# Optimization experiments

Hardware: AMD Instinct MI355X
Metric: run time of the kernel (lower is better)

## Reference

```python
import jax, jax.numpy as jnp
import numpy as np

B, L, D = 2, 2048, 2048
H, KV, HD = 16, 4, 64  # query heads, kv heads, head_dim
EPS = 1e-6
ROPE_BASE = 10000.0


def setup_inputs() -> dict:
    key = jax.random.key(0)
    k0, k1, k2 = jax.random.split(key, 3)
    x = jax.random.normal(k0, (B, L, D), dtype=jnp.float32)
    W_qkv = jax.random.normal(k1, ((H + 2 * KV) * HD, D), dtype=jnp.float32) * 0.02
    W_out = jax.random.normal(k2, (D, H * HD), dtype=jnp.float32) * 0.02
    q_norm_w = jnp.ones((HD,), dtype=jnp.float32)
    k_norm_w = jnp.ones((HD,), dtype=jnp.float32)
    # causal additive mask (forward's optional `mask` arg)
    mask = jnp.triu(jnp.full((L, L), -1e9, dtype=jnp.float32), k=1)
    return {"x": x, "W_qkv": W_qkv, "W_out": W_out,
            "q_norm_w": q_norm_w, "k_norm_w": k_norm_w, "mask": mask}


def _rms_norm(x, w):
    # normalize over last (head) dim
    var = jnp.mean(x * x, axis=-1, keepdims=True)
    return x * jax.lax.rsqrt(var + EPS) * w


def _rope(x):
    # x: [B, nH, L, HD]; non-traditional (rotate-half) RoPE, offset=0
    half = HD // 2
    freqs = ROPE_BASE ** (-jnp.arange(0, HD, 2, dtype=jnp.float32) / HD)  # [half]
    theta = jnp.arange(L, dtype=jnp.float32)[:, None] * freqs[None, :]    # [L, half]
    cos, sin = jnp.cos(theta), jnp.sin(theta)
    x1, x2 = x[..., :half], x[..., half:]
    return jnp.concatenate([x1 * cos - x2 * sin, x1 * sin + x2 * cos], axis=-1)


def reference(x, W_qkv, W_out, q_norm_w, k_norm_w, mask):
    # fused QKV projection
    qkv = jnp.einsum("bld,ed->ble", x, W_qkv)                       # [B,L,(H+2KV)*HD]
    qkv = qkv.reshape(B, L, H + 2 * KV, HD).transpose(0, 2, 1, 3)   # [B,nH,L,HD]
    q, k, v = jnp.split(qkv, [H, H + KV], axis=1)
    # per-head QK RMSNorm + RoPE
    q = _rope(_rms_norm(q, q_norm_w))
    k = _rope(_rms_norm(k, k_norm_w))
    # GQA: repeat kv heads to match query heads
    rep = H // KV
    k = jnp.repeat(k, rep, axis=1)
    v = jnp.repeat(v, rep, axis=1)
    scale = HD ** -0.5
    scores = jnp.einsum("bhqd,bhkd->bhqk", q, k) * scale + mask      # [B,H,L,L]
    attn = jax.nn.softmax(scores, axis=-1)
    out = jnp.einsum("bhqk,bhkd->bhqd", attn, v)                     # [B,H,L,HD]
    out = out.transpose(0, 2, 1, 3).reshape(B, L, H * HD)
    return jnp.einsum("ble,de->bld", out, W_out)                     # [B,L,D]
```

## Files before the change

### kernel.cpp

```cpp
#include <hip/hip_runtime.h>
#include <hip/hip_bf16.h>


typedef __bf16 bf16;
typedef bf16 bf16x8 __attribute__((ext_vector_type(8)));
typedef bf16 bf16x4 __attribute__((ext_vector_type(4)));
typedef float f32x4 __attribute__((ext_vector_type(4)));

#define L_SEQ 2048
#define NQH 16
#define NKVH 4

typedef __attribute__((address_space(3))) void lds_void;
typedef const __attribute__((address_space(1))) void glb_void;
__device__ __forceinline__ void async_ld16(const void* g, void* l) {
  __builtin_amdgcn_global_load_lds((glb_void*)g, (lds_void*)l, 16, 0, 0);
}

__global__ __launch_bounds__(256) void cast_bf16(const float* __restrict__ in,
                                                 bf16* __restrict__ out, int n) {
  int i = (blockIdx.x * 256 + threadIdx.x) * 4;
  if (i < n) {
    float4 v = *(const float4*)&in[i];
    bf16x4 o;
    o[0] = (bf16)v.x; o[1] = (bf16)v.y; o[2] = (bf16)v.z; o[3] = (bf16)v.w;
    *(bf16x4*)&out[i] = o;
  }
}


__global__ __launch_bounds__(256)
void gemm_bt64(const bf16* __restrict__ A, const bf16* __restrict__ B,
               float* __restrict__ C, int M, int N, int K) {
  constexpr int ASZ = 128 * 32, BSZ = 64 * 32;
  __shared__ bf16 As[2 * ASZ];
  __shared__ bf16 Bs[2 * BSZ];
  const int tid = threadIdx.x;
  const int lane = tid & 63, w = tid >> 6;
  const int lq = lane & 15, g = lane >> 4;
  const int wr = w >> 1, wc = w & 1;
  const int bx = blockIdx.x, by = blockIdx.y;

  const bf16* gA[2];
  bf16* ldsA[2];
  const bf16* gB0;
  bf16* ldsB0;
#pragma unroll
  for (int c = 0; c < 2; ++c) {
    int slot = c * 256 + tid;
    int row = slot >> 2, ch = slot & 3;
    int sch = ch ^ ((row >> 1) & 3);
    gA[c] = &A[(size_t)(by * 128 + row) * K + sch * 8];
    ldsA[c] = &As[(c * 256 + w * 64) * 8];
  }
  {
    int row = tid >> 2, ch = tid & 3;
    int sch = ch ^ ((row >> 1) & 3);
    gB0 = &B[(size_t)(bx * 64 + row) * K + sch * 8];
    ldsB0 = &Bs[(w * 64) * 8];
  }

  f32x4 acc[4][2] = {};
  const int nk = K >> 5;
  int cur = 0;

#pragma unroll
  for (int c = 0; c < 2; ++c) async_ld16(gA[c], ldsA[c]);
  async_ld16(gB0, ldsB0);
  __syncthreads();
  for (int kt = 0; kt < nk; ++kt) {
    bf16x8 af[4], bfr[2];
#pragma unroll
    for (int i = 0; i < 4; ++i) {
      int ra = wr * 64 + i * 16 + lq;
      af[i] = *(const bf16x8*)&As[cur * ASZ + ra * 32 + (g ^ ((ra >> 1) & 3)) * 8];
    }
#pragma unroll
    for (int j = 0; j < 2; ++j) {
      int rb = wc * 32 + j * 16 + lq;
      bfr[j] = *(const bf16x8*)&Bs[cur * BSZ + rb * 32 + (g ^ ((rb >> 1) & 3)) * 8];
    }
    if (kt + 1 < nk) {
#pragma unroll
      for (int c = 0; c < 2; ++c) async_ld16(gA[c] + (kt + 1) * 32, ldsA[c] + (cur ^ 1) * ASZ);
      async_ld16(gB0 + (kt + 1) * 32, ldsB0 + (cur ^ 1) * BSZ);
    }
#pragma unroll
    for (int i = 0; i < 4; ++i)
#pragma unroll
      for (int j = 0; j < 2; ++j)
        acc[i][j] = __builtin_amdgcn_mfma_f32_16x16x32_bf16(af[i], bfr[j], acc[i][j], 0, 0, 0);
    __syncthreads();
    cur ^= 1;
  }
#pragma unroll
  for (int i = 0; i < 4; ++i)
#pragma unroll
    for (int j = 0; j < 2; ++j) {
      int row = by * 128 + wr * 64 + i * 16 + g * 4;
      int col = bx * 64 + wc * 32 + j * 16 + lq;
#pragma unroll
      for (int r = 0; r < 4; ++r) C[(size_t)(row + r) * N + col] = acc[i][j][r];
    }
}

__global__ __launch_bounds__(256)
void gemm_qkv_fused(const bf16* __restrict__ A, const bf16* __restrict__ B,
                    const float* __restrict__ qw, const float* __restrict__ kw,
                    bf16* __restrict__ Qb, bf16* __restrict__ Kb,
                    bf16* __restrict__ Vt) {
  constexpr int K = 2048;
  constexpr int ASZ = 128 * 32, BSZ = 64 * 32;
  extern __shared__ char smem[];
  bf16* As = (bf16*)smem;
  bf16* Bs = (bf16*)(smem + 2 * ASZ * 2);
  float* F = (float*)smem;
  const int tid = threadIdx.x;
  const int lane = tid & 63, w = tid >> 6;
  const int lq = lane & 15, g = lane >> 4;
  const int wr = w >> 1, wc = w & 1;
  const int bx = blockIdx.x, by = blockIdx.y;

  const bf16* gA[2];
  bf16* ldsA[2];
  const bf16* gB0;
  bf16* ldsB0;
#pragma unroll
  for (int c = 0; c < 2; ++c) {
    int slot = c * 256 + tid;
    int row = slot >> 2, ch = slot & 3;
    int sch = ch ^ ((row >> 1) & 3);
    gA[c] = &A[(size_t)(by * 128 + row) * K + sch * 8];
    ldsA[c] = &As[(c * 256 + w * 64) * 8];
  }
  {
    int row = tid >> 2, ch = tid & 3;
    int sch = ch ^ ((row >> 1) & 3);
    gB0 = &B[(size_t)(bx * 64 + row) * K + sch * 8];
    ldsB0 = &Bs[(w * 64) * 8];
  }

  f32x4 acc[4][2] = {};
  constexpr int nk = K >> 5;
  int cur = 0;

#pragma unroll
  for (int c = 0; c < 2; ++c) async_ld16(gA[c], ldsA[c]);
  async_ld16(gB0, ldsB0);
  __syncthreads();
  for (int kt = 0; kt < nk; ++kt) {
    bf16x8 af[4], bfr[2];
#pragma unroll
    for (int i = 0; i < 4; ++i) {
      int ra = wr * 64 + i * 16 + lq;
      af[i] = *(const bf16x8*)&As[cur * ASZ + ra * 32 + (g ^ ((ra >> 1) & 3)) * 8];
    }
#pragma unroll
    for (int j = 0; j < 2; ++j) {
      int rb = wc * 32 + j * 16 + lq;
      bfr[j] = *(const bf16x8*)&Bs[cur * BSZ + rb * 32 + (g ^ ((rb >> 1) & 3)) * 8];
    }
    if (kt + 1 < nk) {
#pragma unroll
      for (int c = 0; c < 2; ++c) async_ld16(gA[c] + (kt + 1) * 32, ldsA[c] + (cur ^ 1) * ASZ);
      async_ld16(gB0 + (kt + 1) * 32, ldsB0 + (cur ^ 1) * BSZ);
    }
#pragma unroll
    for (int i = 0; i < 4; ++i)
#pragma unroll
      for (int j = 0; j < 2; ++j)
        acc[i][j] = __builtin_amdgcn_mfma_f32_16x16x32_bf16(af[i], bfr[j], acc[i][j], 0, 0, 0);
    __syncthreads();
    cur ^= 1;
  }

#pragma unroll
  for (int i = 0; i < 4; ++i)
#pragma unroll
    for (int j = 0; j < 2; ++j) {
      int row = wr * 64 + i * 16 + g * 4;
      int col = wc * 32 + j * 16 + lq;
#pragma unroll
      for (int r = 0; r < 4; ++r) F[(row + r) * 66 + col] = acc[i][j][r];
    }
  __syncthreads();

  const int h = bx;
  const int b = by >> 4;
  const int l0 = (by & 15) * 128;

  if (h < 20) {
    const int row = tid >> 1;
    const int half = tid & 1;
    const float* Fr = &F[row * 66];
    float ss = 0.f;
#pragma unroll
    for (int c = 0; c < 32; ++c) {
      float v = Fr[half * 32 + c];
      ss += v * v;
    }
    ss += __shfl_xor(ss, 1);
    const float rs = rsqrtf(ss * (1.f / 64.f) + 1e-6f);
    const int l = l0 + row;
    const float* wn = (h < 16) ? qw : kw;
    const float scale = (h < 16) ? 0.125f : 1.f;
    bf16 lo[16], hi[16];
#pragma unroll
    for (int k = 0; k < 16; ++k) {
      int c = half * 16 + k;
      float x1 = Fr[c] * rs * wn[c];
      float x2 = Fr[c + 32] * rs * wn[c + 32];
      float theta = (float)l * exp2f(-(float)c * 0.41524101186280154f);
      float sn, cs;
      sincosf(theta, &sn, &cs);
      lo[k] = (bf16)((x1 * cs - x2 * sn) * scale);
      hi[k] = (bf16)((x1 * sn + x2 * cs) * scale);
    }
    bf16* dst = (h < 16) ? &Qb[((size_t)(b * NQH + h) * L_SEQ + l) * 64]
                         : &Kb[((size_t)(b * NKVH + (h - 16)) * L_SEQ + l) * 64];
    *(bf16x8*)&dst[half * 16] = *(bf16x8*)&lo[0];
    *(bf16x8*)&dst[half * 16 + 8] = *(bf16x8*)&lo[8];
    *(bf16x8*)&dst[half * 16 + 32] = *(bf16x8*)&hi[0];
    *(bf16x8*)&dst[half * 16 + 40] = *(bf16x8*)&hi[8];
  } else {
    const int d = tid >> 2;
    const int lg = (tid & 3) * 32;
    bf16 tv[32];
#pragma unroll
    for (int jj = 0; jj < 32; ++jj) tv[jj] = (bf16)F[(lg + jj) * 66 + d];
    bf16* dst = &Vt[(size_t)(b * NKVH + (h - 20)) * 64 * L_SEQ + (size_t)d * L_SEQ + l0 + lg];
#pragma unroll
    for (int c = 0; c < 4; ++c) *(bf16x8*)&dst[c * 8] = *(bf16x8*)&tv[c * 8];
  }
}

__global__ __launch_bounds__(256)
void attn(const bf16* __restrict__ Qb, const bf16* __restrict__ Kb,
          const bf16* __restrict__ Vt, bf16* __restrict__ Ao) {
  const int pair = blockIdx.x;
  const int bh = blockIdx.y;
  const int b = bh >> 4, h = bh & 15, kv = h >> 2;
  const int tid = threadIdx.x;
  const int w = tid >> 6, lane = tid & 63;
  const int lq = lane & 15, g = lane >> 4;

  __shared__ bf16 Ks[64][64];
  __shared__ bf16 Vs[64][64];
  __shared__ bf16 Plds[4][16][72];

  const bf16* Qp = Qb + (size_t)(b * NQH + h) * L_SEQ * 64;
  const bf16* Kp = Kb + (size_t)(b * NKVH + kv) * L_SEQ * 64;
  const bf16* Vp = Vt + (size_t)(b * NKVH + kv) * 64 * L_SEQ;

  const int sr0 = tid >> 3, sc = tid & 7;
  const int sr1 = sr0 + 32;
  const int swc0 = (sc ^ (sr0 & 7)) * 8;
  bf16x8 rk0, rk1, rv0, rv1;

  auto load_tile = [&](int k0) {
    rk0 = *(const bf16x8*)&Kp[(size_t)(k0 + sr0) * 64 + sc * 8];
    rk1 = *(const bf16x8*)&Kp[(size_t)(k0 + sr1) * 64 + sc * 8];
    rv0 = *(const bf16x8*)&Vp[(size_t)sr0 * L_SEQ + k0 + sc * 8];
    rv1 = *(const bf16x8*)&Vp[(size_t)sr1 * L_SEQ + k0 + sc * 8];
  };
  auto write_tile = [&]() {
    *(bf16x8*)&Ks[sr0][swc0] = rk0;
    *(bf16x8*)&Ks[sr1][swc0] = rk1;
    *(bf16x8*)&Vs[sr0][swc0] = rv0;
    *(bf16x8*)&Vs[sr1][swc0] = rv1;
  };

  const float L2E = 1.4426950408889634f;

  for (int half = 0; half < 2; ++half) {
    const int qblk = half ? (31 - pair) : pair;
    const int qr0 = qblk * 64 + w * 16;
    const int qg = qr0 + lq;

    bf16x8 qf[2];
    qf[0] = *(const bf16x8*)&Qp[(qr0 + lq) * 64 + g * 8];
    qf[1] = *(const bf16x8*)&Qp[(qr0 + lq) * 64 + 32 + g * 8];

    f32x4 o[4] = {};
    float m = -1e30f, lsum = 0.f;

    const int nkt = qblk + 1;
    load_tile(0);
    __syncthreads();
    write_tile();
    __syncthreads();

    for (int kt = 0; kt < nkt; ++kt) {
      const int k0 = kt * 64;
      const bool diag = (kt == nkt - 1);
      if (kt + 1 < nkt) load_tile(k0 + 64);

      f32x4 s[4] = {};
#pragma unroll
      for (int ks = 0; ks < 4; ++ks) {
        if (!diag || ks <= w) {
          const int row = ks * 16 + lq, sw = lq & 7;
          bf16x8 kf0 = *(const bf16x8*)&Ks[row][(g ^ sw) * 8];
          bf16x8 kf1 = *(const bf16x8*)&Ks[row][((g + 4) ^ sw) * 8];
          s[ks] = __builtin_amdgcn_mfma_f32_16x16x32_bf16(kf0, qf[0], s[ks], 0, 0, 0);
          s[ks] = __builtin_amdgcn_mfma_f32_16x16x32_bf16(kf1, qf[1], s[ks], 0, 0, 0);
        }
      }
      if (diag) {
#pragma unroll
        for (int ks = 0; ks < 4; ++ks)
#pragma unroll
          for (int r = 0; r < 4; ++r)
            if (k0 + ks * 16 + g * 4 + r > qg) s[ks][r] = -1e30f;
      }
      float tmax = -1e30f;
#pragma unroll
      for (int ks = 0; ks < 4; ++ks)
#pragma unroll
        for (int r = 0; r < 4; ++r) tmax = fmaxf(tmax, s[ks][r]);
      tmax = fmaxf(tmax, __shfl_xor(tmax, 16));
      tmax = fmaxf(tmax, __shfl_xor(tmax, 32));
      float mnew = fmaxf(m, tmax);
      float alpha = exp2f((m - mnew) * L2E);
      m = mnew;
      float rsum = 0.f;
#pragma unroll
      for (int ks = 0; ks < 4; ++ks) {
        bf16x4 p;
#pragma unroll
        for (int r = 0; r < 4; ++r) {
          float pv = exp2f((s[ks][r] - mnew) * L2E);
          rsum += pv;
          p[r] = (bf16)pv;
        }
        *(bf16x4*)&Plds[w][lq][ks * 16 + g * 4] = p;
      }
      rsum += __shfl_xor(rsum, 16);
      rsum += __shfl_xor(rsum, 32);
      lsum = lsum * alpha + rsum;

      float ar[4];
#pragma unroll
      for (int r = 0; r < 4; ++r) ar[r] = __shfl(alpha, (lane & 48) | (g * 4 + r));
#pragma unroll
      for (int dt = 0; dt < 4; ++dt)
#pragma unroll
        for (int r = 0; r < 4; ++r) o[dt][r] *= ar[r];

      bf16x8 pf0 = *(const bf16x8*)&Plds[w][lq][g * 8];
      bf16x8 pf1 = *(const bf16x8*)&Plds[w][lq][32 + g * 8];
#pragma unroll
      for (int dt = 0; dt < 4; ++dt) {
        const int row = dt * 16 + lq, sw = lq & 7;
        bf16x8 vf0 = *(const bf16x8*)&Vs[row][(g ^ sw) * 8];
        o[dt] = __builtin_amdgcn_mfma_f32_16x16x32_bf16(pf0, vf0, o[dt], 0, 0, 0);
        if (!diag || w >= 2) {
          bf16x8 vf1 = *(const bf16x8*)&Vs[row][((g + 4) ^ sw) * 8];
          o[dt] = __builtin_amdgcn_mfma_f32_16x16x32_bf16(pf1, vf1, o[dt], 0, 0, 0);
        }
      }

      if (kt + 1 < nkt) {
        __syncthreads();
        write_tile();
        __syncthreads();
      }
    }

    float linv = 1.f / lsum;
#pragma unroll
    for (int r = 0; r < 4; ++r) {
      float li = __shfl(linv, (lane & 48) | (g * 4 + r));
      int row = b * L_SEQ + qr0 + g * 4 + r;
#pragma unroll
      for (int dt = 0; dt < 4; ++dt)
        Ao[(size_t)row * 1024 + h * 64 + dt * 16 + lq] = (bf16)(o[dt][r] * li);
    }
  }
}

extern "C" void kernel_launch(void* const* d_in, const int* in_sizes, int n_in,
                              void* d_out, int out_size, void* d_ws, size_t ws_size,
                              hipStream_t stream) {
  const float* x = (const float*)d_in[0];
  const float* Wqkv = (const float*)d_in[1];
  const float* Wout = (const float*)d_in[2];
  const float* qw = (const float*)d_in[3];
  const float* kw = (const float*)d_in[4];
  float* out = (float*)d_out;

  char* ws = (char*)d_ws;
  size_t off = 0;
  auto alloc = [&](size_t bytes) {
    void* p = ws + off;
    off = (off + bytes + 255) & ~(size_t)255;
    return p;
  };
  bf16* xb = (bf16*)alloc(8388608ull * 2);
  bf16* wqb = (bf16*)alloc(3145728ull * 2);
  bf16* wob = (bf16*)alloc(2097152ull * 2);
  bf16* Qb = (bf16*)alloc(4194304ull * 2);
  bf16* Kb = (bf16*)alloc(1048576ull * 2);
  bf16* Vt = (bf16*)alloc(1048576ull * 2);
  bf16* Ao = (bf16*)alloc(4194304ull * 2);

  cast_bf16<<<8192, 256, 0, stream>>>(x, xb, 8388608);
  cast_bf16<<<3072, 256, 0, stream>>>(Wqkv, wqb, 3145728);
  cast_bf16<<<2048, 256, 0, stream>>>(Wout, wob, 2097152);
  gemm_qkv_fused<<<dim3(24, 32), 256, 33792, stream>>>(xb, wqb, qw, kw, Qb, Kb, Vt);
  attn<<<dim3(16, 32), 256, 0, stream>>>(Qb, Kb, Vt, Ao);
  gemm_bt64<<<dim3(32, 32), 256, 0, stream>>>(Ao, wob, out, 4096, 2048, 1024);
}
```

Measured before the change: 271.9 us.

## Fuse fp32-to-bf16 casts into GEMM loaders and double-buffer attention K/V tiles

Removes the three standalone cast kernels: the QKV and output GEMMs now load fp32 operands into registers, convert to bf16 and store into swizzled LDS, double-buffered around the MFMA loop. The attention kernel gets double-buffered K/V LDS tiles, so each iteration needs one barrier instead of two. This drops the cast launches and the bf16 intermediate round trip. In exchange the GEMMs re-read fp32 data, twice the bytes per tile, and lose the async global-to-LDS path.

```diff
diff --git a/kernel.cpp b/kernel.cpp
--- a/kernel.cpp
+++ b/kernel.cpp
@@ -17,95 +17,15 @@
   __builtin_amdgcn_global_load_lds((glb_void*)g, (lds_void*)l, 16, 0, 0);
 }
 
-__global__ __launch_bounds__(256) void cast_bf16(const float* __restrict__ in,
-                                                 bf16* __restrict__ out, int n) {
-  int i = (blockIdx.x * 256 + threadIdx.x) * 4;
-  if (i < n) {
-    float4 v = *(const float4*)&in[i];
-    bf16x4 o;
-    o[0] = (bf16)v.x; o[1] = (bf16)v.y; o[2] = (bf16)v.z; o[3] = (bf16)v.w;
-    *(bf16x4*)&out[i] = o;
-  }
-}
-
+__device__ __forceinline__ bf16x8 cvt8(const float4& a, const float4& b) {
+  bf16x8 v;
+  v[0] = (bf16)a.x; v[1] = (bf16)a.y; v[2] = (bf16)a.z; v[3] = (bf16)a.w;
+  v[4] = (bf16)b.x; v[5] = (bf16)b.y; v[6] = (bf16)b.z; v[7] = (bf16)b.w;
+  return v;
+}
 
 __global__ __launch_bounds__(256)
-void gemm_bt64(const bf16* __restrict__ A, const bf16* __restrict__ B,
-               float* __restrict__ C, int M, int N, int K) {
-  constexpr int ASZ = 128 * 32, BSZ = 64 * 32;
-  __shared__ bf16 As[2 * ASZ];
-  __shared__ bf16 Bs[2 * BSZ];
-  const int tid = threadIdx.x;
-  const int lane = tid & 63, w = tid >> 6;
-  const int lq = lane & 15, g = lane >> 4;
-  const int wr = w >> 1, wc = w & 1;
-  const int bx = blockIdx.x, by = blockIdx.y;
-
-  const bf16* gA[2];
-  bf16* ldsA[2];
-  const bf16* gB0;
-  bf16* ldsB0;
-#pragma unroll
-  for (int c = 0; c < 2; ++c) {
-    int slot = c * 256 + tid;
-    int row = slot >> 2, ch = slot & 3;
-    int sch = ch ^ ((row >> 1) & 3);
-    gA[c] = &A[(size_t)(by * 128 + row) * K + sch * 8];
-    ldsA[c] = &As[(c * 256 + w * 64) * 8];
-  }
-  {
-    int row = tid >> 2, ch = tid & 3;
-    int sch = ch ^ ((row >> 1) & 3);
-    gB0 = &B[(size_t)(bx * 64 + row) * K + sch * 8];
-    ldsB0 = &Bs[(w * 64) * 8];
-  }
-
-  f32x4 acc[4][2] = {};
-  const int nk = K >> 5;
-  int cur = 0;
-
-#pragma unroll
-  for (int c = 0; c < 2; ++c) async_ld16(gA[c], ldsA[c]);
-  async_ld16(gB0, ldsB0);
-  __syncthreads();
-  for (int kt = 0; kt < nk; ++kt) {
-    bf16x8 af[4], bfr[2];
-#pragma unroll
-    for (int i = 0; i < 4; ++i) {
-      int ra = wr * 64 + i * 16 + lq;
-      af[i] = *(const bf16x8*)&As[cur * ASZ + ra * 32 + (g ^ ((ra >> 1) & 3)) * 8];
-    }
-#pragma unroll
-    for (int j = 0; j < 2; ++j) {
-      int rb = wc * 32 + j * 16 + lq;
-      bfr[j] = *(const bf16x8*)&Bs[cur * BSZ + rb * 32 + (g ^ ((rb >> 1) & 3)) * 8];
-    }
-    if (kt + 1 < nk) {
-#pragma unroll
-      for (int c = 0; c < 2; ++c) async_ld16(gA[c] + (kt + 1) * 32, ldsA[c] + (cur ^ 1) * ASZ);
-      async_ld16(gB0 + (kt + 1) * 32, ldsB0 + (cur ^ 1) * BSZ);
-    }
-#pragma unroll
-    for (int i = 0; i < 4; ++i)
-#pragma unroll
-      for (int j = 0; j < 2; ++j)
-        acc[i][j] = __builtin_amdgcn_mfma_f32_16x16x32_bf16(af[i], bfr[j], acc[i][j], 0, 0, 0);
-    __syncthreads();
-    cur ^= 1;
-  }
-#pragma unroll
-  for (int i = 0; i < 4; ++i)
-#pragma unroll
-    for (int j = 0; j < 2; ++j) {
-      int row = by * 128 + wr * 64 + i * 16 + g * 4;
-      int col = bx * 64 + wc * 32 + j * 16 + lq;
-#pragma unroll
-      for (int r = 0; r < 4; ++r) C[(size_t)(row + r) * N + col] = acc[i][j][r];
-    }
-}
-
-__global__ __launch_bounds__(256)
-void gemm_qkv_fused(const bf16* __restrict__ A, const bf16* __restrict__ B,
+void gemm_qkv_fused(const float* __restrict__ A32, const float* __restrict__ B32,
                     const float* __restrict__ qw, const float* __restrict__ kw,
                     bf16* __restrict__ Qb, bf16* __restrict__ Kb,
                     bf16* __restrict__ Vt) {
@@ -121,32 +41,36 @@
   const int wr = w >> 1, wc = w & 1;
   const int bx = blockIdx.x, by = blockIdx.y;
 
-  const bf16* gA[2];
-  bf16* ldsA[2];
-  const bf16* gB0;
-  bf16* ldsB0;
-#pragma unroll
-  for (int c = 0; c < 2; ++c) {
-    int slot = c * 256 + tid;
-    int row = slot >> 2, ch = slot & 3;
-    int sch = ch ^ ((row >> 1) & 3);
-    gA[c] = &A[(size_t)(by * 128 + row) * K + sch * 8];
-    ldsA[c] = &As[(c * 256 + w * 64) * 8];
-  }
-  {
-    int row = tid >> 2, ch = tid & 3;
-    int sch = ch ^ ((row >> 1) & 3);
-    gB0 = &B[(size_t)(bx * 64 + row) * K + sch * 8];
-    ldsB0 = &Bs[(w * 64) * 8];
-  }
+  const int sch = tid & 3;
+  const int srowA = tid >> 2;
+  const int srowB = tid >> 2;
+  const float* gA0 = &A32[(size_t)(by * 128 + srowA) * K + sch * 8];
+  const float* gA1 = &A32[(size_t)(by * 128 + 64 + srowA) * K + sch * 8];
+  const float* gB0 = &B32[(size_t)(bx * 64 + srowB) * K + sch * 8];
+  const int pchA = (sch ^ ((srowA >> 1) & 3)) * 8;
+  const int pchB = (sch ^ ((srowB >> 1) & 3)) * 8;
+
+  float4 ra0[2], ra1[2], rb[2];
+  auto load_regs = [&](int kt) {
+    const float* p0 = gA0 + kt * 32;
+    ra0[0] = *(const float4*)p0; ra0[1] = *(const float4*)(p0 + 4);
+    const float* p1 = gA1 + kt * 32;
+    ra1[0] = *(const float4*)p1; ra1[1] = *(const float4*)(p1 + 4);
+    const float* pb = gB0 + kt * 32;
+    rb[0] = *(const float4*)pb; rb[1] = *(const float4*)(pb + 4);
+  };
+  auto cvt_write = [&](int buf) {
+    *(bf16x8*)&As[buf * ASZ + srowA * 32 + pchA] = cvt8(ra0[0], ra0[1]);
+    *(bf16x8*)&As[buf * ASZ + (64 + srowA) * 32 + pchA] = cvt8(ra1[0], ra1[1]);
+    *(bf16x8*)&Bs[buf * BSZ + srowB * 32 + pchB] = cvt8(rb[0], rb[1]);
+  };
 
   f32x4 acc[4][2] = {};
   constexpr int nk = K >> 5;
   int cur = 0;
 
-#pragma unroll
-  for (int c = 0; c < 2; ++c) async_ld16(gA[c], ldsA[c]);
-  async_ld16(gB0, ldsB0);
+  load_regs(0);
+  cvt_write(0);
   __syncthreads();
   for (int kt = 0; kt < nk; ++kt) {
     bf16x8 af[4], bfr[2];
@@ -157,19 +81,16 @@
     }
 #pragma unroll
     for (int j = 0; j < 2; ++j) {
-      int rb = wc * 32 + j * 16 + lq;
-      bfr[j] = *(const bf16x8*)&Bs[cur * BSZ + rb * 32 + (g ^ ((rb >> 1) & 3)) * 8];
-    }
-    if (kt + 1 < nk) {
-#pragma unroll
-      for (int c = 0; c < 2; ++c) async_ld16(gA[c] + (kt + 1) * 32, ldsA[c] + (cur ^ 1) * ASZ);
-      async_ld16(gB0 + (kt + 1) * 32, ldsB0 + (cur ^ 1) * BSZ);
-    }
+      int rbr = wc * 32 + j * 16 + lq;
+      bfr[j] = *(const bf16x8*)&Bs[cur * BSZ + rbr * 32 + (g ^ ((rbr >> 1) & 3)) * 8];
+    }
+    if (kt + 1 < nk) load_regs(kt + 1);
 #pragma unroll
     for (int i = 0; i < 4; ++i)
 #pragma unroll
       for (int j = 0; j < 2; ++j)
         acc[i][j] = __builtin_amdgcn_mfma_f32_16x16x32_bf16(af[i], bfr[j], acc[i][j], 0, 0, 0);
+    if (kt + 1 < nk) cvt_write(cur ^ 1);
     __syncthreads();
     cur ^= 1;
   }
@@ -235,6 +156,82 @@
 }
 
 __global__ __launch_bounds__(256)
+void gemm_out(const bf16* __restrict__ A, const float* __restrict__ B32,
+              float* __restrict__ C, int M, int N, int K) {
+  constexpr int ASZ = 128 * 32, BSZ = 64 * 32;
+  __shared__ bf16 As[2 * ASZ];
+  __shared__ bf16 Bs[2 * BSZ];
+  const int tid = threadIdx.x;
+  const int lane = tid & 63, w = tid >> 6;
+  const int lq = lane & 15, g = lane >> 4;
+  const int wr = w >> 1, wc = w & 1;
+  const int bx = blockIdx.x, by = blockIdx.y;
+
+  const bf16* gA[2];
+  bf16* ldsA[2];
+#pragma unroll
+  for (int c = 0; c < 2; ++c) {
+    int slot = c * 256 + tid;
+    int row = slot >> 2, ch = slot & 3;
+    int sch = ch ^ ((row >> 1) & 3);
+    gA[c] = &A[(size_t)(by * 128 + row) * K + sch * 8];
+    ldsA[c] = &As[(c * 256 + w * 64) * 8];
+  }
+  const int sch = tid & 3;
+  const int srowB = tid >> 2;
+  const float* gB0 = &B32[(size_t)(bx * 64 + srowB) * K + sch * 8];
+  const int pchB = (sch ^ ((srowB >> 1) & 3)) * 8;
+  float4 rb[2];
+
+  f32x4 acc[4][2] = {};
+  const int nk = K >> 5;
+  int cur = 0;
+
+#pragma unroll
+  for (int c = 0; c < 2; ++c) async_ld16(gA[c], ldsA[c]);
+  rb[0] = *(const float4*)gB0; rb[1] = *(const float4*)(gB0 + 4);
+  *(bf16x8*)&Bs[srowB * 32 + pchB] = cvt8(rb[0], rb[1]);
+  __syncthreads();
+  for (int kt = 0; kt < nk; ++kt) {
+    bf16x8 af[4], bfr[2];
+#pragma unroll
+    for (int i = 0; i < 4; ++i) {
+      int ra = wr * 64 + i * 16 + lq;
+      af[i] = *(const bf16x8*)&As[cur * ASZ + ra * 32 + (g ^ ((ra >> 1) & 3)) * 8];
+    }
+#pragma unroll
+    for (int j = 0; j < 2; ++j) {
+      int rbr = wc * 32 + j * 16 + lq;
+      bfr[j] = *(const bf16x8*)&Bs[cur * BSZ + rbr * 32 + (g ^ ((rbr >> 1) & 3)) * 8];
+    }
+    if (kt + 1 < nk) {
+#pragma unroll
+      for (int c = 0; c < 2; ++c) async_ld16(gA[c] + (kt + 1) * 32, ldsA[c] + (cur ^ 1) * ASZ);
+      const float* pb = gB0 + (kt + 1) * 32;
+      rb[0] = *(const float4*)pb; rb[1] = *(const float4*)(pb + 4);
+    }
+#pragma unroll
+    for (int i = 0; i < 4; ++i)
+#pragma unroll
+      for (int j = 0; j < 2; ++j)
+        acc[i][j] = __builtin_amdgcn_mfma_f32_16x16x32_bf16(af[i], bfr[j], acc[i][j], 0, 0, 0);
+    if (kt + 1 < nk)
+      *(bf16x8*)&Bs[(cur ^ 1) * BSZ + srowB * 32 + pchB] = cvt8(rb[0], rb[1]);
+    __syncthreads();
+    cur ^= 1;
+  }
+#pragma unroll
+  for (int i = 0; i < 4; ++i)
+#pragma unroll
+    for (int j = 0; j < 2; ++j) {
+      int row = by * 128 + wr * 64 + i * 16 + g * 4;
+      int col = bx * 64 + wc * 32 + j * 16 + lq;
+#pragma unroll
+      for (int r = 0; r < 4; ++r) C[(size_t)(row + r) * N + col] = acc[i][j][r];
+    }
+}
+
+__global__ __launch_bounds__(256)
 void attn(const bf16* __restrict__ Qb, const bf16* __restrict__ Kb,
           const bf16* __restrict__ Vt, bf16* __restrict__ Ao) {
   const int pair = blockIdx.x;
@@ -244,8 +241,8 @@
   const int w = tid >> 6, lane = tid & 63;
   const int lq = lane & 15, g = lane >> 4;
 
-  __shared__ bf16 Ks[64][64];
-  __shared__ bf16 Vs[64][64];
+  __shared__ bf16 Ks[2][64][64];
+  __shared__ bf16 Vs[2][64][64];
   __shared__ bf16 Plds[4][16][72];
 
   const bf16* Qp = Qb + (size_t)(b * NQH + h) * L_SEQ * 64;
@@ -263,11 +260,11 @@
     rv0 = *(const bf16x8*)&Vp[(size_t)sr0 * L_SEQ + k0 + sc * 8];
     rv1 = *(const bf16x8*)&Vp[(size_t)sr1 * L_SEQ + k0 + sc * 8];
   };
-  auto write_tile = [&]() {
-    *(bf16x8*)&Ks[sr0][swc0] = rk0;
-    *(bf16x8*)&Ks[sr1][swc0] = rk1;
-    *(bf16x8*)&Vs[sr0][swc0] = rv0;
-    *(bf16x8*)&Vs[sr1][swc0] = rv1;
+  auto write_tile = [&](int buf) {
+    *(bf16x8*)&Ks[buf][sr0][swc0] = rk0;
+    *(bf16x8*)&Ks[buf][sr1][swc0] = rk1;
+    *(bf16x8*)&Vs[buf][sr0][swc0] = rv0;
+    *(bf16x8*)&Vs[buf][sr1][swc0] = rv1;
   };
 
   const float L2E = 1.4426950408889634f;
@@ -285,9 +282,10 @@
     float m = -1e30f, lsum = 0.f;
 
     const int nkt = qblk + 1;
+    int cur = 0;
     load_tile(0);
     __syncthreads();
-    write_tile();
+    write_tile(0);
     __syncthreads();
 
     for (int kt = 0; kt < nkt; ++kt) {
@@ -300,8 +298,8 @@
       for (int ks = 0; ks < 4; ++ks) {
         if (!diag || ks <= w) {
           const int row = ks * 16 + lq, sw = lq & 7;
-          bf16x8 kf0 = *(const bf16x8*)&Ks[row][(g ^ sw) * 8];
-          bf16x8 kf1 = *(const bf16x8*)&Ks[row][((g + 4) ^ sw) * 8];
+          bf16x8 kf0 = *(const bf16x8*)&Ks[cur][row][(g ^ sw) * 8];
+          bf16x8 kf1 = *(const bf16x8*)&Ks[cur][row][((g + 4) ^ sw) * 8];
           s[ks] = __builtin_amdgcn_mfma_f32_16x16x32_bf16(kf0, qf[0], s[ks], 0, 0, 0);
           s[ks] = __builtin_amdgcn_mfma_f32_16x16x32_bf16(kf1, qf[1], s[ks], 0, 0, 0);
         }
@@ -352,19 +350,17 @@
 #pragma unroll
       for (int dt = 0; dt < 4; ++dt) {
         const int row = dt * 16 + lq, sw = lq & 7;
-        bf16x8 vf0 = *(const bf16x8*)&Vs[row][(g ^ sw) * 8];
+        bf16x8 vf0 = *(const bf16x8*)&Vs[cur][row][(g ^ sw) * 8];
         o[dt] = __builtin_amdgcn_mfma_f32_16x16x32_bf16(pf0, vf0, o[dt], 0, 0, 0);
         if (!diag || w >= 2) {
-          bf16x8 vf1 = *(const bf16x8*)&Vs[row][((g + 4) ^ sw) * 8];
+          bf16x8 vf1 = *(const bf16x8*)&Vs[cur][row][((g + 4) ^ sw) * 8];
           o[dt] = __builtin_amdgcn_mfma_f32_16x16x32_bf16(pf1, vf1, o[dt], 0, 0, 0);
         }
       }
 
-      if (kt + 1 < nkt) {
-        __syncthreads();
-        write_tile();
-        __syncthreads();
-      }
+      if (kt + 1 < nkt) write_tile(cur ^ 1);
+      __syncthreads();
+      cur ^= 1;
     }
 
     float linv = 1.f / lsum;
@@ -396,18 +392,12 @@
     off = (off + bytes + 255) & ~(size_t)255;
     return p;
   };
-  bf16* xb = (bf16*)alloc(8388608ull * 2);
-  bf16* wqb = (bf16*)alloc(3145728ull * 2);
-  bf16* wob = (bf16*)alloc(2097152ull * 2);
   bf16* Qb = (bf16*)alloc(4194304ull * 2);
   bf16* Kb = (bf16*)alloc(1048576ull * 2);
   bf16* Vt = (bf16*)alloc(1048576ull * 2);
   bf16* Ao = (bf16*)alloc(4194304ull * 2);
 
-  cast_bf16<<<8192, 256, 0, stream>>>(x, xb, 8388608);
-  cast_bf16<<<3072, 256, 0, stream>>>(Wqkv, wqb, 3145728);
-  cast_bf16<<<2048, 256, 0, stream>>>(Wout, wob, 2097152);
-  gemm_qkv_fused<<<dim3(24, 32), 256, 33792, stream>>>(xb, wqb, qw, kw, Qb, Kb, Vt);
+  gemm_qkv_fused<<<dim3(24, 32), 256, 33792, stream>>>(x, Wqkv, qw, kw, Qb, Kb, Vt);
   attn<<<dim3(16, 32), 256, 0, stream>>>(Qb, Kb, Vt, Ao);
-  gemm_bt64<<<dim3(32, 32), 256, 0, stream>>>(Ao, wob, out, 4096, 2048, 1024);
-}
+  gemm_out<<<dim3(32, 32), 256, 0, stream>>>(Ao, Wout, out, 4096, 2048, 1024);
+}
```

New measurement: 267.8 us. Within noise of the previous version (-1.5%).
